# Kernel optimization log

Hardware: AMD Instinct MI355X
Metric: run time of the kernel (lower is better)

The kernel has to match this reference:

```python
import jax, jax.numpy as jnp
import numpy as np

N = 40000    # nodes
E = 500000   # edges
B = 512      # graphs
NEG_SLOPE = 0.2


def setup_inputs() -> dict:
    key = jax.random.key(0)
    ks = jax.random.split(key, 32)
    p = lambda i, shape: jax.random.normal(ks[i], shape, jnp.float32) * 0.1
    return dict(
        x=jax.random.normal(ks[0], (N, 4), jnp.float32),
        edge_index=jax.random.randint(ks[1], (2, E), 0, N),
        edge_attr=jax.random.normal(ks[2], (E, 1), jnp.float32),
        batch=jnp.sort(jax.random.randint(ks[3], (N,), 0, B)),
        w0=p(4, (1, 4)), b0=p(5, (4,)),
        wl1=p(6, (7, 256)), wr1=p(7, (7, 256)), we1=p(8, (1, 256)), att1=p(9, (8, 32)), b1=p(10, (256,)),
        wl2=p(11, (256, 128)), wr2=p(12, (256, 128)), we2=p(13, (1, 128)), att2=p(14, (8, 16)), b2=p(15, (128,)),
        wl3=p(16, (128, 8)), wr3=p(17, (128, 8)), we3=p(18, (1, 8)), att3=p(19, (1, 8)), b3=p(20, (8,)),
        w4=p(21, (8, 1)), b4=p(22, (1,)),
    )


def _gatv2(x, src, dst, ea, wl, wr, we, att, bias, heads, ch):
    # GATv2Conv: score = att . leaky_relu(Wl x_src + Wr x_dst + We e), segment softmax over dst
    n = x.shape[0]
    xl = (x @ wl).reshape(n, heads, ch)      # source transform [n,H,C]
    xr = (x @ wr).reshape(n, heads, ch)      # target transform
    ee = (ea @ we).reshape(-1, heads, ch)    # edge transform   [Ef,H,C]
    s = jax.nn.leaky_relu(xl[src] + xr[dst] + ee, NEG_SLOPE)
    logits = jnp.einsum('ehc,hc->eh', s, att)
    m = jax.lax.stop_gradient(jax.ops.segment_max(logits, dst, num_segments=n))
    ex = jnp.exp(logits - m[dst])
    denom = jax.ops.segment_sum(ex, dst, num_segments=n)
    alpha = ex / denom[dst]                  # softmax over incoming edges of each node
    out = jax.ops.segment_sum(alpha[:, :, None] * xl[src], dst, num_segments=n)
    return out.reshape(n, heads * ch) + bias


def _forward(x, edge_index, edge_attr, batch,
             w0, b0, wl1, wr1, we1, att1, b1, wl2, wr2, we2, att2, b2,
             wl3, wr3, we3, att3, b3, w4, b4):
    src, dst = edge_index[0], edge_index[1]
    n = x.shape[0]
    # add self loops (PyG default, fill_value='mean' = mean of incoming edge_attr)
    deg = jax.ops.segment_sum(jnp.ones((src.shape[0],), jnp.float32), dst, num_segments=n)
    esum = jax.ops.segment_sum(edge_attr, dst, num_segments=n)
    loop_attr = jnp.where(deg[:, None] > 0, esum / jnp.maximum(deg, 1.0)[:, None], 0.0)
    idx = jnp.arange(n)
    src_f = jnp.concatenate([src, idx])
    dst_f = jnp.concatenate([dst, idx])
    ea_f = jnp.concatenate([edge_attr, loop_attr], axis=0)
    # embed atom type, keep xyz -> 7 features
    h = jnp.concatenate([x[:, :1] @ w0 + b0, x[:, 1:]], axis=1)
    h = jnp.tanh(_gatv2(h, src_f, dst_f, ea_f, wl1, wr1, we1, att1, b1, 8, 32))
    # dropout(p=0.6) is identity in eval mode
    h = jnp.tanh(_gatv2(h, src_f, dst_f, ea_f, wl2, wr2, we2, att2, b2, 8, 16))
    h = jnp.tanh(_gatv2(h, src_f, dst_f, ea_f, wl3, wr3, we3, att3, b3, 1, 8))
    # scatter-mean pooling per graph
    cnt = jax.ops.segment_sum(jnp.ones((n,), jnp.float32), batch, num_segments=B)
    pooled = jax.ops.segment_sum(h, batch, num_segments=B) / jnp.maximum(cnt, 1.0)[:, None]
    return pooled @ w4 + b4  # [B,1]


def reference(x, edge_index, edge_attr, batch, w0, b0, wl1, wr1, we1, att1, b1,
              wl2, wr2, we2, att2, b2, wl3, wr3, we3, att3, b3, w4, b4):
    return _forward(x, edge_index, edge_attr, batch, w0, b0, wl1, wr1, we1, att1, b1,
                    wl2, wr2, we2, att2, b2, wl3, wr3, we3, att3, b3, w4, b4)
```

## Files before the change

kernel.cpp:

```cpp
#include <hip/hip_runtime.h>
#include <math.h>

#define NN 40000
#define NNP 40192
#define NE 500000
#define NEF (NN + NE)
#define NB 512
#define NEG 0.2f

static inline int cdiv(int a, int b) { return (a + b - 1) / b; }

typedef __attribute__((ext_vector_type(8))) short short8;
typedef __attribute__((ext_vector_type(4))) short short4v;
typedef __attribute__((ext_vector_type(4))) float f32x4;
typedef __attribute__((ext_vector_type(2))) _Float16 half2v;

__device__ __forceinline__ unsigned short f2bf(float f) {
  unsigned u = __float_as_uint(f);
  unsigned r = (u + 0x7fffu + ((u >> 16) & 1u)) >> 16;
  return (unsigned short)r;
}
__device__ __forceinline__ float bf2f(unsigned short h) {
  return __uint_as_float((unsigned)h << 16);
}
__device__ __forceinline__ float lrelu(float v) {
  return fmaxf(v, NEG * v);
}
__device__ __forceinline__ float red8(float p) {
  p += __uint_as_float((unsigned)__builtin_amdgcn_mov_dpp((int)__float_as_uint(p), 0xB1, 0xF, 0xF, true));
  p += __uint_as_float((unsigned)__builtin_amdgcn_mov_dpp((int)__float_as_uint(p), 0x4E, 0xF, 0xF, true));
  p += __uint_as_float((unsigned)__builtin_amdgcn_mov_dpp((int)__float_as_uint(p), 0x141, 0xF, 0xF, true));
  return p;
}

__global__ void k_deg(const int* __restrict__ ei, const float* __restrict__ ea,
                      int* __restrict__ degi, float* __restrict__ esum) {
  int e = blockIdx.x * 256 + threadIdx.x;
  if (e < NE) {
    int d = ei[NE + e];
    atomicAdd(degi + d, 1);
    atomicAdd(esum + d, ea[e]);
  }
}

__global__ void k_scanA(const int* __restrict__ degi, int* __restrict__ pre,
                        int* __restrict__ bsum, float* __restrict__ lpa) {
  __shared__ int sh[256];
  int t = threadIdx.x, i = blockIdx.x * 256 + t;
  int dg = i < NN ? degi[i] : -1;
  sh[t] = i < NN ? dg + 1 : 0;
  if (i < NN) lpa[i] = dg > 0 ? lpa[i] / (float)dg : 0.f;
  __syncthreads();
  for (int st = 1; st < 256; st <<= 1) {
    int a = t >= st ? sh[t - st] : 0;
    __syncthreads();
    sh[t] += a;
    __syncthreads();
  }
  if (i < NN) pre[i] = sh[t];
  if (t == 255) bsum[blockIdx.x] = sh[255];
}

__global__ void k_scan2(int* __restrict__ bsum, int nb) {
  __shared__ int sh[256];
  int t = threadIdx.x;
  sh[t] = t < nb ? bsum[t] : 0;
  __syncthreads();
  for (int st = 1; st < 256; st <<= 1) {
    int a = t >= st ? sh[t - st] : 0;
    __syncthreads();
    sh[t] += a;
    __syncthreads();
  }
  if (t < nb) bsum[t] = sh[t];
}

__global__ void k_scan3(const int* __restrict__ pre, const int* __restrict__ bsum,
                        int* __restrict__ rowptr) {
  int i = blockIdx.x * 256 + threadIdx.x;
  if (i < NN) {
    int off = blockIdx.x > 0 ? bsum[blockIdx.x - 1] : 0;
    rowptr[i + 1] = pre[i] + off;
    if (i == 0) rowptr[0] = 0;
  }
}

__global__ void k_fill(const int* __restrict__ ei, const float* __restrict__ ea,
                       const float* __restrict__ lpa, const int* __restrict__ rowptr,
                       int* __restrict__ fillc, int* __restrict__ csrc,
                       float* __restrict__ ceav) {
  int e = blockIdx.x * 256 + threadIdx.x;
  if (e >= NEF) return;
  int s, d;
  float v;
  if (e < NE) { s = ei[e]; d = ei[NE + e]; v = ea[e]; }
  else        { s = e - NE; d = s; v = lpa[s]; }
  int pos = atomicAdd(fillc + d, 1);
  int idx = rowptr[d] + pos;
  csrc[idx] = s;
  ceav[idx] = v;
}

__global__ __launch_bounds__(256) void k_gat1(const int* __restrict__ rowptr,
                                              const int* __restrict__ csrc,
                                              const float* __restrict__ ceav,
                                              const float* __restrict__ xx,
                                              const float* __restrict__ w0,
                                              const float* __restrict__ b0,
                                              const float* __restrict__ wl,
                                              const float* __restrict__ wr,
                                              const float* __restrict__ we,
                                              const float* __restrict__ att,
                                              const float* __restrict__ bias,
                                              short* __restrict__ ah,
                                              short* __restrict__ al) {
  const int lane = threadIdx.x & 63;
  const int node = __builtin_amdgcn_readfirstlane(blockIdx.x * 4 + (threadIdx.x >> 6));
  const int j0 = lane * 4;
  if (node >= NN) {
    short4v z = {0, 0, 0, 0};
    *(short4v*)(ah + (size_t)node * 256 + j0) = z;
    *(short4v*)(al + (size_t)node * 256 + j0) = z;
    return;
  }

  float4 wev = *(const float4*)(we + j0);
  float4 attv = *(const float4*)(att + j0);
  float w0s[4] = {w0[0], w0[1], w0[2], w0[3]};
  float b0s[4] = {b0[0], b0[1], b0[2], b0[3]};
  float u[4] = {0.f, 0.f, 0.f, 0.f}, v[4] = {0.f, 0.f, 0.f, 0.f};
#pragma unroll
  for (int j = 0; j < 4; j++) {
    float4 t = *(const float4*)(wl + j * 256 + j0);
    float tt[4] = {t.x, t.y, t.z, t.w};
#pragma unroll
    for (int c = 0; c < 4; c++) {
      u[c] = fmaf(w0s[j], tt[c], u[c]);
      v[c] = fmaf(b0s[j], tt[c], v[c]);
    }
  }
  float4 wl4 = *(const float4*)(wl + 4 * 256 + j0);
  float4 wl5 = *(const float4*)(wl + 5 * 256 + j0);
  float4 wl6 = *(const float4*)(wl + 6 * 256 + j0);

  float xrr[4] = {0.f, 0.f, 0.f, 0.f};
  {
    float4 xv = *(const float4*)(xx + (size_t)node * 4);
    float hn[7] = {fmaf(xv.x, w0s[0], b0s[0]), fmaf(xv.x, w0s[1], b0s[1]),
                   fmaf(xv.x, w0s[2], b0s[2]), fmaf(xv.x, w0s[3], b0s[3]),
                   xv.y, xv.z, xv.w};
#pragma unroll
    for (int k = 0; k < 7; k++) {
      float4 t = *(const float4*)(wr + k * 256 + j0);
      xrr[0] = fmaf(hn[k], t.x, xrr[0]);
      xrr[1] = fmaf(hn[k], t.y, xrr[1]);
      xrr[2] = fmaf(hn[k], t.z, xrr[2]);
      xrr[3] = fmaf(hn[k], t.w, xrr[3]);
    }
  }

  float m = -INFINITY, den = 0.f;
  float acc[4] = {0.f, 0.f, 0.f, 0.f};
  const int kb = rowptr[node], ke = rowptr[node + 1];

#define G1_EDGE(XS, EAV)                                                        \
  {                                                                             \
    float xls[4];                                                               \
    _Pragma("unroll")                                                           \
    for (int c = 0; c < 4; c++) xls[c] = fmaf((XS).x, u[c], v[c]);              \
    xls[0] = fmaf((XS).y, wl4.x, xls[0]); xls[1] = fmaf((XS).y, wl4.y, xls[1]); \
    xls[2] = fmaf((XS).y, wl4.z, xls[2]); xls[3] = fmaf((XS).y, wl4.w, xls[3]); \
    xls[0] = fmaf((XS).z, wl5.x, xls[0]); xls[1] = fmaf((XS).z, wl5.y, xls[1]); \
    xls[2] = fmaf((XS).z, wl5.z, xls[2]); xls[3] = fmaf((XS).z, wl5.w, xls[3]); \
    xls[0] = fmaf((XS).w, wl6.x, xls[0]); xls[1] = fmaf((XS).w, wl6.y, xls[1]); \
    xls[2] = fmaf((XS).w, wl6.z, xls[2]); xls[3] = fmaf((XS).w, wl6.w, xls[3]); \
    float p = 0.f;                                                              \
    p = fmaf(lrelu(xls[0] + fmaf((EAV), wev.x, xrr[0])), attv.x, p);            \
    p = fmaf(lrelu(xls[1] + fmaf((EAV), wev.y, xrr[1])), attv.y, p);            \
    p = fmaf(lrelu(xls[2] + fmaf((EAV), wev.z, xrr[2])), attv.z, p);            \
    p = fmaf(lrelu(xls[3] + fmaf((EAV), wev.w, xrr[3])), attv.w, p);            \
    p = red8(p);                                                                \
    if (!__all(p <= m + 8.f)) {                                                 \
      float mn = fmaxf(m, p);                                                   \
      float sc = __expf(m - mn);                                                \
      den *= sc;                                                                \
      _Pragma("unroll")                                                         \
      for (int c = 0; c < 4; c++) acc[c] *= sc;                                 \
      m = mn;                                                                   \
    }                                                                           \
    float ex = __expf(p - m);                                                   \
    den += ex;                                                                  \
    _Pragma("unroll")                                                           \
    for (int c = 0; c < 4; c++) acc[c] = fmaf(ex, xls[c], acc[c]);              \
  }

  int i1 = kb + 1 < ke ? kb + 1 : ke - 1;
  float eA = ceav[kb], eB = ceav[i1];
  float4 xA = *(const float4*)(xx + (size_t)csrc[kb] * 4);
  float4 xB = *(const float4*)(xx + (size_t)csrc[i1] * 4);
  for (int k = kb; k < ke; k += 2) {
    const int i2 = k + 2 < ke ? k + 2 : ke - 1;
    const int i3 = k + 3 < ke ? k + 3 : ke - 1;
    const float eC = ceav[i2], eD = ceav[i3];
    const float4 xC = *(const float4*)(xx + (size_t)csrc[i2] * 4);
    const float4 xD = *(const float4*)(xx + (size_t)csrc[i3] * 4);
    G1_EDGE(xA, eA);
    if (k + 1 < ke) {
      G1_EDGE(xB, eB);
    }
    xA = xC; eA = eC; xB = xD; eB = eD;
  }
#undef G1_EDGE

  float rd = 1.f / den;
  float4 bv = *(const float4*)(bias + j0);
  float bb[4] = {bv.x, bv.y, bv.z, bv.w};
  short hi[4], lo[4];
#pragma unroll
  for (int c = 0; c < 4; c++) {
    float hv = tanhf(fmaf(acc[c], rd, bb[c]));
    unsigned short hb = f2bf(hv);
    hi[c] = (short)hb;
    lo[c] = (short)f2bf(hv - bf2f(hb));
  }
  *(short4v*)(ah + (size_t)node * 256 + j0) = *(short4v*)hi;
  *(short4v*)(al + (size_t)node * 256 + j0) = *(short4v*)lo;
}

__global__ void k_wsplit(const float* __restrict__ wl, const float* __restrict__ wr,
                         short* __restrict__ bh, short* __restrict__ bl) {
  int id = blockIdx.x * 256 + threadIdx.x;
  int n = id >> 8, k = id & 255;
  float w = n < 128 ? wl[k * 128 + n] : wr[k * 128 + n - 128];
  unsigned short hb = f2bf(w);
  bh[n * 256 + k] = (short)hb;
  bl[n * 256 + k] = (short)f2bf(w - bf2f(hb));
}

__global__ __launch_bounds__(256) void k_gemm2(const short* __restrict__ ah,
                                               const short* __restrict__ al,
                                               const short* __restrict__ bh,
                                               const short* __restrict__ bl,
                                               _Float16* __restrict__ xlh,
                                               float* __restrict__ xr) {
  __shared__ short sAh[256 * 40];
  __shared__ short sAl[256 * 40];
  __shared__ short sBh[64 * 40];
  __shared__ short sBl[64 * 40];
  const int tid = threadIdx.x;
  const int bm = blockIdx.x >> 2, bn = blockIdx.x & 3;
  const int wid = tid >> 6, lane = tid & 63;
  const int wr = wid >> 1, wc = wid & 1;
  const int l15 = lane & 15, lhi = lane >> 4;
  const int srow = tid >> 2;
  const int kq = (tid & 3) * 8;
  f32x4 acc[8][2];
#pragma unroll
  for (int a = 0; a < 8; a++)
#pragma unroll
    for (int b = 0; b < 2; b++) acc[a][b] = (f32x4)(0.f);

#pragma unroll 1
  for (int st = 0; st < 8; st++) {
    const int k0 = st * 32;
    short8 vh[4], vl[4], vbh, vbl;
#pragma unroll
    for (int ps = 0; ps < 4; ps++) {
      const long off = (long)(bm * 256 + ps * 64 + srow) * 256 + k0 + kq;
      vh[ps] = *(const short8*)(ah + off);
      vl[ps] = *(const short8*)(al + off);
    }
    {
      const long boff = (long)(bn * 64 + srow) * 256 + k0 + kq;
      vbh = *(const short8*)(bh + boff);
      vbl = *(const short8*)(bl + boff);
    }
    __syncthreads();
#pragma unroll
    for (int ps = 0; ps < 4; ps++) {
      *(short8*)&sAh[(ps * 64 + srow) * 40 + kq] = vh[ps];
      *(short8*)&sAl[(ps * 64 + srow) * 40 + kq] = vl[ps];
    }
    *(short8*)&sBh[srow * 40 + kq] = vbh;
    *(short8*)&sBl[srow * 40 + kq] = vbl;
    __syncthreads();
    short8 bfh[2], bfl[2];
#pragma unroll
    for (int fn = 0; fn < 2; fn++) {
      bfh[fn] = *(const short8*)&sBh[(wc * 32 + fn * 16 + l15) * 40 + lhi * 8];
      bfl[fn] = *(const short8*)&sBl[(wc * 32 + fn * 16 + l15) * 40 + lhi * 8];
    }
#pragma unroll
    for (int fm = 0; fm < 8; fm++) {
      short8 afh = *(const short8*)&sAh[(wr * 128 + fm * 16 + l15) * 40 + lhi * 8];
      short8 afl = *(const short8*)&sAl[(wr * 128 + fm * 16 + l15) * 40 + lhi * 8];
      acc[fm][0] = __builtin_amdgcn_mfma_f32_16x16x32_bf16(afh, bfh[0], acc[fm][0], 0, 0, 0);
      acc[fm][1] = __builtin_amdgcn_mfma_f32_16x16x32_bf16(afh, bfh[1], acc[fm][1], 0, 0, 0);
      acc[fm][0] = __builtin_amdgcn_mfma_f32_16x16x32_bf16(afh, bfl[0], acc[fm][0], 0, 0, 0);
      acc[fm][1] = __builtin_amdgcn_mfma_f32_16x16x32_bf16(afh, bfl[1], acc[fm][1], 0, 0, 0);
      acc[fm][0] = __builtin_amdgcn_mfma_f32_16x16x32_bf16(afl, bfh[0], acc[fm][0], 0, 0, 0);
      acc[fm][1] = __builtin_amdgcn_mfma_f32_16x16x32_bf16(afl, bfh[1], acc[fm][1], 0, 0, 0);
    }
  }
#pragma unroll
  for (int fm = 0; fm < 8; fm++)
#pragma unroll
    for (int fn = 0; fn < 2; fn++) {
      int col = bn * 64 + wc * 32 + fn * 16 + l15;
#pragma unroll
      for (int j = 0; j < 4; j++) {
        int row = bm * 256 + wr * 128 + fm * 16 + lhi * 4 + j;
        if (col < 128) xlh[(long)row * 128 + col] = (_Float16)acc[fm][fn][j];
        else           xr[(long)row * 128 + col - 128] = acc[fm][fn][j];
      }
    }
}

__global__ __launch_bounds__(256) void k_gat2(const int* __restrict__ rowptr,
                                              const int* __restrict__ csrc,
                                              const float* __restrict__ ceav,
                                              const _Float16* __restrict__ xlh,
                                              const float* __restrict__ xr,
                                              const float* __restrict__ we,
                                              const float* __restrict__ att,
                                              const float* __restrict__ bias,
                                              float* __restrict__ hout) {
  const int lane = threadIdx.x & 63;
  const int node = __builtin_amdgcn_readfirstlane(blockIdx.x * 4 + (threadIdx.x >> 6));
  if (node >= NN) return;
  const int j0 = lane * 2;
  float2 xrr = *(const float2*)(xr + (long)node * 128 + j0);
  float2 wev = *(const float2*)(we + j0);
  float2 attv = *(const float2*)(att + j0);
  float m = -INFINITY, den = 0.f, acc0 = 0.f, acc1 = 0.f;
  const int kb = rowptr[node], ke = rowptr[node + 1];

#define G2_EDGE(AV, EAV)                                                  \
  {                                                                       \
    float av0 = (float)(AV).x, av1 = (float)(AV).y;                       \
    float v0 = lrelu(av0 + fmaf((EAV), wev.x, xrr.x));                    \
    float v1 = lrelu(av1 + fmaf((EAV), wev.y, xrr.y));                    \
    float p = red8(fmaf(v0, attv.x, v1 * attv.y));                        \
    if (!__all(p <= m + 8.f)) {                                           \
      float mn = fmaxf(m, p);                                             \
      float sc = __expf(m - mn);                                          \
      den *= sc;                                                          \
      acc0 *= sc;                                                         \
      acc1 *= sc;                                                         \
      m = mn;                                                             \
    }                                                                     \
    float ex = __expf(p - m);                                             \
    den += ex;                                                            \
    acc0 = fmaf(ex, av0, acc0);                                           \
    acc1 = fmaf(ex, av1, acc1);                                           \
  }

  int i1 = kb + 1 < ke ? kb + 1 : ke - 1;
  float eA = ceav[kb], eB = ceav[i1];
  half2v aA = *(const half2v*)(xlh + (long)csrc[kb] * 128 + j0);
  half2v aB = *(const half2v*)(xlh + (long)csrc[i1] * 128 + j0);
  for (int k = kb; k < ke; k += 2) {
    const int i2 = k + 2 < ke ? k + 2 : ke - 1;
    const int i3 = k + 3 < ke ? k + 3 : ke - 1;
    const float eC = ceav[i2], eD = ceav[i3];
    const half2v aC = *(const half2v*)(xlh + (long)csrc[i2] * 128 + j0);
    const half2v aD = *(const half2v*)(xlh + (long)csrc[i3] * 128 + j0);
    G2_EDGE(aA, eA);
    if (k + 1 < ke) {
      G2_EDGE(aB, eB);
    }
    aA = aC; eA = eC; aB = aD; eB = eD;
  }
#undef G2_EDGE

  float rd = 1.f / den;
  hout[(long)node * 128 + j0]     = tanhf(fmaf(acc0, rd, bias[j0]));
  hout[(long)node * 128 + j0 + 1] = tanhf(fmaf(acc1, rd, bias[j0 + 1]));
}

__global__ __launch_bounds__(256) void k_mm3(const float* __restrict__ h,
                                             const float* __restrict__ wl,
                                             const float* __restrict__ wr,
                                             float* __restrict__ xl,
                                             float* __restrict__ xr) {
  __shared__ float srow[64 * 132];
  __shared__ float lw[128 * 16];
  const int t = threadIdx.x;
  const int n0 = blockIdx.x * 64;
#pragma unroll
  for (int q = 0; q < 8; q++) {
    int gi = (t + q * 256) * 4;
    int row = gi >> 7, col = gi & 127;
    float4 v = *(const float4*)(h + (size_t)(n0 + row) * 128 + col);
    *(float4*)&srow[row * 132 + col] = v;
  }
#pragma unroll
  for (int q = 0; q < 8; q++) {
    int idx = t + q * 256;
    int k = idx >> 4, j = idx & 15;
    lw[idx] = j < 8 ? wl[k * 8 + j] : wr[k * 8 + (j - 8)];
  }
  __syncthreads();
  const int nid = t >> 2, g = t & 3;
  float a0 = 0.f, a1 = 0.f, a2 = 0.f, a3 = 0.f;
  const float* rp = &srow[nid * 132];
  for (int k = 0; k < 128; k++) {
    float hv = rp[k];
    float4 w = *(const float4*)&lw[k * 16 + g * 4];
    a0 = fmaf(hv, w.x, a0);
    a1 = fmaf(hv, w.y, a1);
    a2 = fmaf(hv, w.z, a2);
    a3 = fmaf(hv, w.w, a3);
  }
  float4 r = {a0, a1, a2, a3};
  int node = n0 + nid;
  float* dst = (g & 2) ? xr : xl;
  *(float4*)(dst + node * 8 + (g & 1) * 4) = r;
}

__global__ __launch_bounds__(256) void k_gat3(const int* __restrict__ rowptr,
                                              const int* __restrict__ csrc,
                                              const float* __restrict__ ceav,
                                              const float* __restrict__ xl,
                                              const float* __restrict__ xr,
                                              const float* __restrict__ we,
                                              const float* __restrict__ att,
                                              const float* __restrict__ bias,
                                              float* __restrict__ hout) {
  const int lane = threadIdx.x & 7;
  const int node = blockIdx.x * 32 + (threadIdx.x >> 3);
  if (node >= NN) return;
  const float xrr = xr[node * 8 + lane];
  const float wev = we[lane];
  const float attv = att[lane];
  float m = -INFINITY, den = 0.f, acc = 0.f;
  const int kb = rowptr[node], ke = rowptr[node + 1];
  for (int k = kb; k < ke; k++) {
    const int s = csrc[k];
    const float eav = ceav[k];
    const float av = xl[s * 8 + lane];
    float v = lrelu(av + fmaf(eav, wev, xrr));
    float p = red8(v * attv);
    if (p > m + 8.f) {
      float mn = fmaxf(m, p);
      float sc = __expf(m - mn);
      den *= sc;
      acc *= sc;
      m = mn;
    }
    float ex = __expf(p - m);
    den += ex;
    acc = fmaf(ex, av, acc);
  }
  hout[node * 8 + lane] = tanhf(acc / den + bias[lane]);
}

__global__ void k_gbound(const int* __restrict__ bat, int* __restrict__ gstart) {
  int i = blockIdx.x * 256 + threadIdx.x;
  if (i >= NN) return;
  int b = bat[i];
  int bp = i > 0 ? bat[i - 1] : -1;
  for (int g = bp + 1; g <= b; g++) gstart[g] = i;
  if (i == NN - 1)
    for (int g = b + 1; g <= NB; g++) gstart[g] = NN;
}

__global__ __launch_bounds__(256) void k_poolG(const int* __restrict__ gstart,
                                               const float* __restrict__ h3,
                                               const float* __restrict__ w4,
                                               const float* __restrict__ b4,
                                               float* __restrict__ out) {
  const int lane = threadIdx.x & 63;
  const int g = blockIdx.x * 4 + (threadIdx.x >> 6);
  if (g >= NB) return;
  const int kb = gstart[g], ke = gstart[g + 1];
  const int ch = lane & 7, no = lane >> 3;
  float acc = 0.f;
  for (int n = kb + no; n < ke; n += 8)
    acc += h3[(size_t)n * 8 + ch];
  acc += __shfl_xor(acc, 8);
  acc += __shfl_xor(acc, 16);
  acc += __shfl_xor(acc, 32);
  float cnt = fmaxf((float)(ke - kb), 1.f);
  float yv = (acc / cnt) * w4[ch];
  yv = red8(yv);
  if (lane == 0) out[g] = yv + b4[0];
}

extern "C" void kernel_launch(void* const* d_in, const int* in_sizes, int n_in,
                              void* d_out, int out_size, void* d_ws, size_t ws_size,
                              hipStream_t stream) {
  const float* x   = (const float*)d_in[0];
  const int*   ei  = (const int*)d_in[1];
  const float* ea  = (const float*)d_in[2];
  const int*   bat = (const int*)d_in[3];
  const float* w0  = (const float*)d_in[4];
  const float* b0  = (const float*)d_in[5];
  const float* wl1 = (const float*)d_in[6];
  const float* wr1 = (const float*)d_in[7];
  const float* we1 = (const float*)d_in[8];
  const float* at1 = (const float*)d_in[9];
  const float* b1  = (const float*)d_in[10];
  const float* wl2 = (const float*)d_in[11];
  const float* wr2 = (const float*)d_in[12];
  const float* we2 = (const float*)d_in[13];
  const float* at2 = (const float*)d_in[14];
  const float* b2  = (const float*)d_in[15];
  const float* wl3 = (const float*)d_in[16];
  const float* wr3 = (const float*)d_in[17];
  const float* we3 = (const float*)d_in[18];
  const float* at3 = (const float*)d_in[19];
  const float* b3  = (const float*)d_in[20];
  const float* w4  = (const float*)d_in[21];
  const float* b4  = (const float*)d_in[22];
  float* out = (float*)d_out;

  char* W = (char*)d_ws;
  size_t o = 0;
  auto alloc = [&](size_t bytes) { void* p = W + o; o += (bytes + 255) & ~(size_t)255; return p; };
  int*      degi   = (int*)alloc(NN * 4);
  int*      fillc  = (int*)alloc(NN * 4);
  float*    lpa    = (float*)alloc(NN * 4);
  int*      rowptr = (int*)alloc((NN + 1) * 4);
  int*      pre    = (int*)alloc(NN * 4);
  int*      bsum   = (int*)alloc(256 * 4);
  int*      gstart = (int*)alloc((NB + 1) * 4);
  int*      csrc   = (int*)alloc((size_t)NEF * 4);
  float*    ceav   = (float*)alloc((size_t)NEF * 4);
  short*    Ah     = (short*)alloc((size_t)NNP * 256 * 2);
  short*    Al     = (short*)alloc((size_t)NNP * 256 * 2);
  short*    Bh     = (short*)alloc((size_t)256 * 256 * 2);
  short*    Bl     = (short*)alloc((size_t)256 * 256 * 2);
  _Float16* Xlh2   = (_Float16*)alloc((size_t)NNP * 128 * 2);
  float*    Xr2    = (float*)alloc((size_t)NNP * 128 * 4);
  float*    H2     = (float*)alloc((size_t)NN * 128 * 4);
  float*    Xl3    = (float*)alloc((size_t)NN * 8 * 4);
  float*    Xr3    = (float*)alloc((size_t)NN * 8 * 4);
  float*    H3     = (float*)alloc((size_t)NN * 8 * 4);
  (void)ws_size; (void)in_sizes; (void)n_in; (void)out_size;

  const int NBLK = cdiv(NN, 256);

  hipMemsetAsync(degi, 0, 3 * NN * 4, stream);
  k_deg<<<cdiv(NE, 256), 256, 0, stream>>>(ei, ea, degi, lpa);
  k_scanA<<<NBLK, 256, 0, stream>>>(degi, pre, bsum, lpa);
  k_scan2<<<1, 256, 0, stream>>>(bsum, NBLK);
  k_scan3<<<NBLK, 256, 0, stream>>>(pre, bsum, rowptr);
  k_fill<<<cdiv(NEF, 256), 256, 0, stream>>>(ei, ea, lpa, rowptr, fillc, csrc, ceav);
  k_gbound<<<NBLK, 256, 0, stream>>>(bat, gstart);

  k_gat1<<<NNP / 4, 256, 0, stream>>>(rowptr, csrc, ceav, x, w0, b0, wl1, wr1, we1, at1, b1, Ah, Al);

  k_wsplit<<<256, 256, 0, stream>>>(wl2, wr2, Bh, Bl);
  k_gemm2<<<(NNP / 256) * 4, 256, 0, stream>>>(Ah, Al, Bh, Bl, Xlh2, Xr2);
  k_gat2<<<cdiv(NN, 4), 256, 0, stream>>>(rowptr, csrc, ceav, Xlh2, Xr2, we2, at2, b2, H2);

  k_mm3<<<NN / 64, 256, 0, stream>>>(H2, wl3, wr3, Xl3, Xr3);
  k_gat3<<<cdiv(NN, 32), 256, 0, stream>>>(rowptr, csrc, ceav, Xl3, Xr3, we3, at3, b3, H3);

  k_poolG<<<cdiv(NB, 4), 256, 0, stream>>>(gstart, H3, w4, b4, out);
}
```

Baseline: 260.0 us.

## Fold graph-boundary and block-scan kernels into neighbours, halve GEMM M tile

The graph-boundary computation moves into the first scan kernel, and the single-block scan of block sums is recomputed redundantly inside every block of the final scan kernel. Together these remove two kernel launches and their serialization gaps. The layer-2 GEMM tile shrinks from 256 to 128 rows per block, doubling the grid for better CU occupancy on a small-M-per-CU problem, at the cost of less B-tile reuse. The redundant per-block scan adds a little work to each block.

```diff
diff --git a/kernel.cpp b/kernel.cpp
--- a/kernel.cpp
+++ b/kernel.cpp
@@ -7,6 +7,7 @@
 #define NEF (NN + NE)
 #define NB 512
 #define NEG 0.2f
+#define NBLK_C 157
 
 static inline int cdiv(int a, int b) { return (a + b - 1) / b; }
 
@@ -44,12 +45,20 @@
 }
 
 __global__ void k_scanA(const int* __restrict__ degi, int* __restrict__ pre,
-                        int* __restrict__ bsum, float* __restrict__ lpa) {
+                        int* __restrict__ bsum, float* __restrict__ lpa,
+                        const int* __restrict__ bat, int* __restrict__ gstart) {
   __shared__ int sh[256];
   int t = threadIdx.x, i = blockIdx.x * 256 + t;
   int dg = i < NN ? degi[i] : -1;
   sh[t] = i < NN ? dg + 1 : 0;
-  if (i < NN) lpa[i] = dg > 0 ? lpa[i] / (float)dg : 0.f;
+  if (i < NN) {
+    lpa[i] = dg > 0 ? lpa[i] / (float)dg : 0.f;
+    int b = bat[i];
+    int bp = i > 0 ? bat[i - 1] : -1;
+    for (int g = bp + 1; g <= b; g++) gstart[g] = i;
+    if (i == NN - 1)
+      for (int g = b + 1; g <= NB; g++) gstart[g] = NN;
+  }
   __syncthreads();
   for (int st = 1; st < 256; st <<= 1) {
     int a = t >= st ? sh[t - st] : 0;
@@ -61,10 +70,11 @@
   if (t == 255) bsum[blockIdx.x] = sh[255];
 }
 
-__global__ void k_scan2(int* __restrict__ bsum, int nb) {
+__global__ void k_scan3(const int* __restrict__ pre, const int* __restrict__ bsum,
+                        int* __restrict__ rowptr) {
   __shared__ int sh[256];
   int t = threadIdx.x;
-  sh[t] = t < nb ? bsum[t] : 0;
+  sh[t] = t < NBLK_C ? bsum[t] : 0;
   __syncthreads();
   for (int st = 1; st < 256; st <<= 1) {
     int a = t >= st ? sh[t - st] : 0;
@@ -72,14 +82,9 @@
     sh[t] += a;
     __syncthreads();
   }
-  if (t < nb) bsum[t] = sh[t];
-}
-
-__global__ void k_scan3(const int* __restrict__ pre, const int* __restrict__ bsum,
-                        int* __restrict__ rowptr) {
-  int i = blockIdx.x * 256 + threadIdx.x;
+  int i = blockIdx.x * 256 + t;
   if (i < NN) {
-    int off = blockIdx.x > 0 ? bsum[blockIdx.x - 1] : 0;
+    int off = blockIdx.x > 0 ? sh[blockIdx.x - 1] : 0;
     rowptr[i + 1] = pre[i] + off;
     if (i == 0) rowptr[0] = 0;
   }
@@ -243,8 +248,8 @@
                                                const short* __restrict__ bl,
                                                _Float16* __restrict__ xlh,
                                                float* __restrict__ xr) {
-  __shared__ short sAh[256 * 40];
-  __shared__ short sAl[256 * 40];
+  __shared__ short sAh[128 * 40];
+  __shared__ short sAl[128 * 40];
   __shared__ short sBh[64 * 40];
   __shared__ short sBl[64 * 40];
   const int tid = threadIdx.x;
@@ -254,33 +259,29 @@
   const int l15 = lane & 15, lhi = lane >> 4;
   const int srow = tid >> 2;
   const int kq = (tid & 3) * 8;
-  f32x4 acc[8][2];
-#pragma unroll
-  for (int a = 0; a < 8; a++)
+  f32x4 acc[4][2];
+#pragma unroll
+  for (int a = 0; a < 4; a++)
 #pragma unroll
     for (int b = 0; b < 2; b++) acc[a][b] = (f32x4)(0.f);
 
 #pragma unroll 1
   for (int st = 0; st < 8; st++) {
     const int k0 = st * 32;
-    short8 vh[4], vl[4], vbh, vbl;
-#pragma unroll
-    for (int ps = 0; ps < 4; ps++) {
-      const long off = (long)(bm * 256 + ps * 64 + srow) * 256 + k0 + kq;
-      vh[ps] = *(const short8*)(ah + off);
-      vl[ps] = *(const short8*)(al + off);
-    }
-    {
-      const long boff = (long)(bn * 64 + srow) * 256 + k0 + kq;
-      vbh = *(const short8*)(bh + boff);
-      vbl = *(const short8*)(bl + boff);
-    }
+    const long aoff0 = (long)(bm * 128 + srow) * 256 + k0 + kq;
+    const long aoff1 = aoff0 + 64 * 256;
+    const long boff = (long)(bn * 64 + srow) * 256 + k0 + kq;
+    short8 vah0 = *(const short8*)(ah + aoff0);
+    short8 vah1 = *(const short8*)(ah + aoff1);
+    short8 val0 = *(const short8*)(al + aoff0);
+    short8 val1 = *(const short8*)(al + aoff1);
+    short8 vbh  = *(const short8*)(bh + boff);
+    short8 vbl  = *(const short8*)(bl + boff);
     __syncthreads();
-#pragma unroll
-    for (int ps = 0; ps < 4; ps++) {
-      *(short8*)&sAh[(ps * 64 + srow) * 40 + kq] = vh[ps];
-      *(short8*)&sAl[(ps * 64 + srow) * 40 + kq] = vl[ps];
-    }
+    *(short8*)&sAh[srow * 40 + kq] = vah0;
+    *(short8*)&sAh[(64 + srow) * 40 + kq] = vah1;
+    *(short8*)&sAl[srow * 40 + kq] = val0;
+    *(short8*)&sAl[(64 + srow) * 40 + kq] = val1;
     *(short8*)&sBh[srow * 40 + kq] = vbh;
     *(short8*)&sBl[srow * 40 + kq] = vbl;
     __syncthreads();
@@ -291,9 +292,9 @@
       bfl[fn] = *(const short8*)&sBl[(wc * 32 + fn * 16 + l15) * 40 + lhi * 8];
     }
 #pragma unroll
-    for (int fm = 0; fm < 8; fm++) {
-      short8 afh = *(const short8*)&sAh[(wr * 128 + fm * 16 + l15) * 40 + lhi * 8];
-      short8 afl = *(const short8*)&sAl[(wr * 128 + fm * 16 + l15) * 40 + lhi * 8];
+    for (int fm = 0; fm < 4; fm++) {
+      short8 afh = *(const short8*)&sAh[(wr * 64 + fm * 16 + l15) * 40 + lhi * 8];
+      short8 afl = *(const short8*)&sAl[(wr * 64 + fm * 16 + l15) * 40 + lhi * 8];
       acc[fm][0] = __builtin_amdgcn_mfma_f32_16x16x32_bf16(afh, bfh[0], acc[fm][0], 0, 0, 0);
       acc[fm][1] = __builtin_amdgcn_mfma_f32_16x16x32_bf16(afh, bfh[1], acc[fm][1], 0, 0, 0);
       acc[fm][0] = __builtin_amdgcn_mfma_f32_16x16x32_bf16(afh, bfl[0], acc[fm][0], 0, 0, 0);
@@ -303,13 +304,13 @@
     }
   }
 #pragma unroll
-  for (int fm = 0; fm < 8; fm++)
+  for (int fm = 0; fm < 4; fm++)
 #pragma unroll
     for (int fn = 0; fn < 2; fn++) {
       int col = bn * 64 + wc * 32 + fn * 16 + l15;
 #pragma unroll
       for (int j = 0; j < 4; j++) {
-        int row = bm * 256 + wr * 128 + fm * 16 + lhi * 4 + j;
+        int row = bm * 128 + wr * 64 + fm * 16 + lhi * 4 + j;
         if (col < 128) xlh[(long)row * 128 + col] = (_Float16)acc[fm][fn][j];
         else           xr[(long)row * 128 + col - 128] = acc[fm][fn][j];
       }
@@ -455,16 +456,6 @@
   hout[node * 8 + lane] = tanhf(acc / den + bias[lane]);
 }
 
-__global__ void k_gbound(const int* __restrict__ bat, int* __restrict__ gstart) {
-  int i = blockIdx.x * 256 + threadIdx.x;
-  if (i >= NN) return;
-  int b = bat[i];
-  int bp = i > 0 ? bat[i - 1] : -1;
-  for (int g = bp + 1; g <= b; g++) gstart[g] = i;
-  if (i == NN - 1)
-    for (int g = b + 1; g <= NB; g++) gstart[g] = NN;
-}
-
 __global__ __launch_bounds__(256) void k_poolG(const int* __restrict__ gstart,
                                                const float* __restrict__ h3,
                                                const float* __restrict__ w4,
@@ -543,16 +534,14 @@
 
   hipMemsetAsync(degi, 0, 3 * NN * 4, stream);
   k_deg<<<cdiv(NE, 256), 256, 0, stream>>>(ei, ea, degi, lpa);
-  k_scanA<<<NBLK, 256, 0, stream>>>(degi, pre, bsum, lpa);
-  k_scan2<<<1, 256, 0, stream>>>(bsum, NBLK);
+  k_scanA<<<NBLK, 256, 0, stream>>>(degi, pre, bsum, lpa, bat, gstart);
   k_scan3<<<NBLK, 256, 0, stream>>>(pre, bsum, rowptr);
   k_fill<<<cdiv(NEF, 256), 256, 0, stream>>>(ei, ea, lpa, rowptr, fillc, csrc, ceav);
-  k_gbound<<<NBLK, 256, 0, stream>>>(bat, gstart);
 
   k_gat1<<<NNP / 4, 256, 0, stream>>>(rowptr, csrc, ceav, x, w0, b0, wl1, wr1, we1, at1, b1, Ah, Al);
 
   k_wsplit<<<256, 256, 0, stream>>>(wl2, wr2, Bh, Bl);
-  k_gemm2<<<(NNP / 256) * 4, 256, 0, stream>>>(Ah, Al, Bh, Bl, Xlh2, Xr2);
+  k_gemm2<<<(NNP / 128) * 4, 256, 0, stream>>>(Ah, Al, Bh, Bl, Xlh2, Xr2);
   k_gat2<<<cdiv(NN, 4), 256, 0, stream>>>(rowptr, csrc, ceav, Xlh2, Xr2, we2, at2, b2, H2);
 
   k_mm3<<<NN / 64, 256, 0, stream>>>(H2, wl3, wr3, Xl3, Xr3);
```

Result: faster. 244.7 us (-5.9%).
